# Kernel tuning notes

Hardware: AMD Instinct MI355X
Metric: run time of the kernel (lower is better)

## Reference

```python
import jax, jax.numpy as jnp
import numpy as np

N = 50000   # in_size (nodes)
E = 400000  # edges per network
H = 4       # n_heads
D = 64      # dimension per head
M = 3       # n_modalities


def setup_inputs() -> dict:
    key = jax.random.key(0)
    ks = jax.random.split(key, 10)
    return {
        "x": jax.random.normal(ks[0], (N, H * D), dtype=jnp.float32),
        "edge_index_0": jax.random.randint(ks[1], (2, E), 0, N, dtype=jnp.int32),
        "edge_index_1": jax.random.randint(ks[2], (2, E), 0, N, dtype=jnp.int32),
        "edge_index_2": jax.random.randint(ks[3], (2, E), 0, N, dtype=jnp.int32),
        "attn_0": jax.random.uniform(ks[4], (E, H), dtype=jnp.float32),
        "attn_1": jax.random.uniform(ks[5], (E, H), dtype=jnp.float32),
        "attn_2": jax.random.uniform(ks[6], (E, H), dtype=jnp.float32),
        "net_weights": jax.random.uniform(ks[7], (M,), dtype=jnp.float32),
        "lin_weight": jax.random.normal(ks[8], (H * D, H * D), dtype=jnp.float32) * (1.0 / np.sqrt(H * D)),
        "bias": jnp.zeros((H * D,), dtype=jnp.float32),
    }


def reference(x, edge_index_0, edge_index_1, edge_index_2,
              attn_0, attn_1, attn_2, net_weights, lin_weight, bias):
    # --- aggregat_edge_weights: per-network scalar weight * per-edge attention,
    # combined into one sparse COO attention matrix. Coalescing (summing duplicate
    # edges) is deferred to the scatter-add below, which is mathematically identical.
    edges = jnp.concatenate([edge_index_0, edge_index_1, edge_index_2], axis=1)  # [2, 3E]
    alpha = jnp.concatenate([
        net_weights[0] * attn_0,
        net_weights[1] * attn_1,
        net_weights[2] * attn_2,
    ], axis=0)  # [3E, H]

    # --- CoAttnWGATConv with precomputed alpha (no self-loops):
    # project, reshape to heads, gather source messages, scale by alpha, scatter-sum.
    xp = (x @ lin_weight).reshape(N, H, D)          # [N, H, D]
    src, dst = edges[0], edges[1]
    msgs = xp[src] * alpha[:, :, None]              # [3E, H, D]
    out = jax.ops.segment_sum(msgs, dst, num_segments=N)  # [N, H, D]
    return out.reshape(N, H * D) + bias
```

## Files before the change

### kernel.cpp

```cpp
#include <hip/hip_runtime.h>

#define N_NODES 50000
#define N_EDGES 400000
#define TOT_E   (3 * N_EDGES)
#define CH      256
#define NHEADS  4
#define BUCKET  64

typedef __attribute__((ext_vector_type(8))) short short8v;
typedef __attribute__((ext_vector_type(8))) unsigned short ushort8v;
typedef __attribute__((ext_vector_type(4))) float float4v;

__device__ inline unsigned short f2b(float f) {
  union { float f; unsigned u; } x; x.f = f;
  return (unsigned short)((x.u + 0x7FFFu + ((x.u >> 16) & 1u)) >> 16);
}
__device__ inline float b2f(unsigned short s) {
  union { unsigned u; float f; } x; x.u = ((unsigned)s) << 16;
  return x.f;
}
__device__ inline float h2f(unsigned short s) {
  return (float)__builtin_bit_cast(_Float16, s);
}

__global__ __launch_bounds__(256) void prep_kernel(
    const float* __restrict__ W, unsigned short* __restrict__ WTp,
    int* __restrict__ cursor) {
  int i = blockIdx.x * 256 + threadIdx.x;
  if (i < N_NODES) cursor[i] = 0;
  if (i < 8192) {
    int f = i >> 9, ks = (i >> 6) & 7, l = i & 63;
    int lr = l & 15, lk = l >> 4;
    unsigned short* dst = WTp + (size_t)i * 8;
    #pragma unroll
    for (int j = 0; j < 8; ++j)
      dst[j] = f2b(W[(ks * 32 + lk * 8 + j) * 256 + f * 16 + lr]);
  }
}

__global__ __launch_bounds__(256) void gemm_kernel(
    const float* __restrict__ x, const unsigned short* __restrict__ WTp,
    unsigned short* __restrict__ xpb) {
  const int tid = threadIdx.x;
  const int w = tid >> 6;
  const int l = tid & 63;
  const int lr = l & 15, lk = l >> 4;
  const int xrow = blockIdx.x * 64 + w * 16 + lr;
  const int fbase = blockIdx.y * 4;
  const bool valid = (xrow < N_NODES);
  const short8v* __restrict__ wp = (const short8v*)WTp;

  float4v acc[4];
  #pragma unroll
  for (int f = 0; f < 4; ++f) acc[f] = (float4v)0.0f;

  for (int ks = 0; ks < 8; ++ks) {
    short8v b;
    if (valid) {
      const float4* px = (const float4*)(x + (size_t)xrow * 256 + ks * 32 + lk * 8);
      float4 u0 = px[0], u1 = px[1];
      b[0]=(short)f2b(u0.x); b[1]=(short)f2b(u0.y); b[2]=(short)f2b(u0.z); b[3]=(short)f2b(u0.w);
      b[4]=(short)f2b(u1.x); b[5]=(short)f2b(u1.y); b[6]=(short)f2b(u1.z); b[7]=(short)f2b(u1.w);
    } else {
      b = (short8v)0;
    }
    #pragma unroll
    for (int f = 0; f < 4; ++f) {
      short8v a = wp[((fbase + f) * 8 + ks) * 64 + l];
      acc[f] = __builtin_amdgcn_mfma_f32_16x16x32_bf16(a, b, acc[f], 0, 0, 0);
    }
  }

  if (valid) {
    unsigned short* rowp = xpb + (size_t)xrow * 256 + lk * 4;
    #pragma unroll
    for (int f = 0; f < 4; ++f) {
      ushort4 pk;
      pk.x = f2b(acc[f][0]);
      pk.y = f2b(acc[f][1]);
      pk.z = f2b(acc[f][2]);
      pk.w = f2b(acc[f][3]);
      *(ushort4*)(rowp + (fbase + f) * 16) = pk;
    }
  }
}

__global__ __launch_bounds__(256) void fill_kernel(
    const int* __restrict__ e0, const int* __restrict__ e1,
    const int* __restrict__ e2,
    const float* __restrict__ a0, const float* __restrict__ a1,
    const float* __restrict__ a2, const float* __restrict__ nw,
    int* __restrict__ cursor, int* __restrict__ srcs,
    ushort4* __restrict__ abuf) {
  int g = blockIdx.x * 256 + threadIdx.x;
  if (g >= TOT_E) return;
  int net = (g >= 2 * N_EDGES) ? 2 : (g >= N_EDGES ? 1 : 0);
  int e = g - net * N_EDGES;
  const int* ei = (net == 0) ? e0 : (net == 1 ? e1 : e2);
  const float* at = (net == 0) ? a0 : (net == 1 ? a1 : a2);
  const float wv = nw[net];
  int src = ei[e];
  int dst = ei[N_EDGES + e];
  float4 al = *(const float4*)(at + (size_t)e * NHEADS);
  ushort4 pk;
  pk.x = __builtin_bit_cast(unsigned short, (_Float16)(wv * al.x));
  pk.y = __builtin_bit_cast(unsigned short, (_Float16)(wv * al.y));
  pk.z = __builtin_bit_cast(unsigned short, (_Float16)(wv * al.z));
  pk.w = __builtin_bit_cast(unsigned short, (_Float16)(wv * al.w));
  int pos = atomicAdd(&cursor[dst], 1);
  if (pos < BUCKET) {
    size_t slot = (size_t)dst * BUCKET + pos;
    srcs[slot] = src;
    abuf[slot] = pk;
  }
}

__global__ __launch_bounds__(256) void gather_kernel(
    const int* __restrict__ srcs, const ushort4* __restrict__ abuf,
    const int* __restrict__ cursor,
    const unsigned short* __restrict__ xpb, const float* __restrict__ bias,
    float* __restrict__ out) {
  const int wid = (blockIdx.x * 256 + threadIdx.x) >> 6;
  const int lane = threadIdx.x & 63;
  const int half = lane >> 5;
  const int l = lane & 31;
  const int n = wid * 2 + half;
  const int c = l * 8;
  const int h = l >> 3;

  const int cnt = min(cursor[n], BUCKET);
  const int* __restrict__ sp = srcs + (size_t)n * BUCKET;
  const ushort4* __restrict__ ap = abuf + (size_t)n * BUCKET;

  float acc[8] = {};
  int i = 0;
  for (; i + 4 <= cnt; i += 4) {
    int4 s4 = *(const int4*)(sp + i);
    ushort8v a01 = *(const ushort8v*)(ap + i);
    ushort8v a23 = *(const ushort8v*)(ap + i + 2);
    float A0 = h2f((unsigned short)a01[h]);
    float A1 = h2f((unsigned short)a01[4 + h]);
    float A2 = h2f((unsigned short)a23[h]);
    float A3 = h2f((unsigned short)a23[4 + h]);
    ushort8v v0 = *(const ushort8v*)(xpb + (size_t)s4.x * CH + c);
    ushort8v v1 = *(const ushort8v*)(xpb + (size_t)s4.y * CH + c);
    ushort8v v2 = *(const ushort8v*)(xpb + (size_t)s4.z * CH + c);
    ushort8v v3 = *(const ushort8v*)(xpb + (size_t)s4.w * CH + c);
    #pragma unroll
    for (int j = 0; j < 8; ++j) {
      acc[j] += A0 * b2f(v0[j]) + A1 * b2f(v1[j]) +
                A2 * b2f(v2[j]) + A3 * b2f(v3[j]);
    }
  }
  for (; i < cnt; ++i) {
    int s = sp[i];
    ushort4 av = ap[i];
    float A = h2f((h & 2) ? ((h & 1) ? av.w : av.z) : ((h & 1) ? av.y : av.x));
    ushort8v v = *(const ushort8v*)(xpb + (size_t)s * CH + c);
    #pragma unroll
    for (int j = 0; j < 8; ++j) acc[j] += A * b2f(v[j]);
  }

  const float4 b0 = *(const float4*)(bias + c);
  const float4 b1 = *(const float4*)(bias + c + 4);
  float* o = out + (size_t)n * CH + c;
  *(float4*)(o + 0) = make_float4(acc[0] + b0.x, acc[1] + b0.y, acc[2] + b0.z, acc[3] + b0.w);
  *(float4*)(o + 4) = make_float4(acc[4] + b1.x, acc[5] + b1.y, acc[6] + b1.z, acc[7] + b1.w);
}

extern "C" void kernel_launch(void* const* d_in, const int* in_sizes, int n_in,
                              void* d_out, int out_size, void* d_ws, size_t ws_size,
                              hipStream_t stream) {
  const float* x    = (const float*)d_in[0];
  const int*   e0   = (const int*)d_in[1];
  const int*   e1   = (const int*)d_in[2];
  const int*   e2   = (const int*)d_in[3];
  const float* a0   = (const float*)d_in[4];
  const float* a1   = (const float*)d_in[5];
  const float* a2   = (const float*)d_in[6];
  const float* nw   = (const float*)d_in[7];
  const float* W    = (const float*)d_in[8];
  const float* bias = (const float*)d_in[9];
  float* out = (float*)d_out;

  char* ws = (char*)d_ws;
  size_t o = 0;
  unsigned short* xpb = (unsigned short*)(ws + o); o += (size_t)N_NODES * CH * 2;
  int* srcs      = (int*)(ws + o);                 o += (size_t)N_NODES * BUCKET * 4;
  ushort4* abuf  = (ushort4*)(ws + o);             o += (size_t)N_NODES * BUCKET * 8;
  unsigned short* WTp = (unsigned short*)(ws + o); o += 65536 * 2;
  int* cursor    = (int*)(ws + o);                 o += (size_t)N_NODES * 4;

  const int nNodeBlk = (N_NODES + 255) / 256;
  const int nEdgeBlk = (TOT_E + 255) / 256;

  prep_kernel<<<nNodeBlk, 256, 0, stream>>>(W, WTp, cursor);
  gemm_kernel<<<dim3((N_NODES + 63) / 64, 4), 256, 0, stream>>>(x, WTp, xpb);
  fill_kernel<<<nEdgeBlk, 256, 0, stream>>>(e0, e1, e2, a0, a1, a2, nw,
                                            cursor, srcs, abuf);
  gather_kernel<<<N_NODES / 8, 256, 0, stream>>>(
      srcs, abuf, cursor, xpb, bias, out);
}
```

Measured before the change: 212.8 us.

## Fuse edge bucketing and projection GEMM into one launch with packed edge records

Merges the edge fill kernel and the bf16 MFMA projection GEMM into a single launch that splits work by block index, so the latency-bound atomic bucketing can overlap with the compute-bound GEMM. Source index and fp16 attention weights are packed into one 16-byte record per slot, so the gather does one vector load per edge instead of separate index and attention loads. Cursor zeroing moves to hipMemsetAsync and the prep kernel shrinks to the weight repack only. In exchange, the record buffer is larger because of a padding word, and the fused blocks differ in register needs, which may reduce occupancy.

```diff
diff --git a/kernel.cpp b/kernel.cpp
--- a/kernel.cpp
+++ b/kernel.cpp
@@ -6,6 +6,9 @@
 #define CH      256
 #define NHEADS  4
 #define BUCKET  64
+
+#define FILL_BLOCKS ((TOT_E + 255) / 256)
+#define GEMM_BLOCKS (((N_NODES + 63) / 64) * 4)
 
 typedef __attribute__((ext_vector_type(8))) short short8v;
 typedef __attribute__((ext_vector_type(8))) unsigned short ushort8v;
@@ -22,102 +25,97 @@
 __device__ inline float h2f(unsigned short s) {
   return (float)__builtin_bit_cast(_Float16, s);
 }
+__device__ inline unsigned short f2h(float f) {
+  return __builtin_bit_cast(unsigned short, (_Float16)f);
+}
 
 __global__ __launch_bounds__(256) void prep_kernel(
-    const float* __restrict__ W, unsigned short* __restrict__ WTp,
-    int* __restrict__ cursor) {
+    const float* __restrict__ W, unsigned short* __restrict__ WTp) {
   int i = blockIdx.x * 256 + threadIdx.x;
-  if (i < N_NODES) cursor[i] = 0;
-  if (i < 8192) {
-    int f = i >> 9, ks = (i >> 6) & 7, l = i & 63;
-    int lr = l & 15, lk = l >> 4;
-    unsigned short* dst = WTp + (size_t)i * 8;
-    #pragma unroll
-    for (int j = 0; j < 8; ++j)
-      dst[j] = f2b(W[(ks * 32 + lk * 8 + j) * 256 + f * 16 + lr]);
-  }
+  int f = i >> 9, ks = (i >> 6) & 7, l = i & 63;
+  int lr = l & 15, lk = l >> 4;
+  unsigned short* dst = WTp + (size_t)i * 8;
+  #pragma unroll
+  for (int j = 0; j < 8; ++j)
+    dst[j] = f2b(W[(ks * 32 + lk * 8 + j) * 256 + f * 16 + lr]);
 }
 
-__global__ __launch_bounds__(256) void gemm_kernel(
+__global__ __launch_bounds__(256) void fused_kernel(
+    const int* __restrict__ e0, const int* __restrict__ e1,
+    const int* __restrict__ e2,
+    const float* __restrict__ a0, const float* __restrict__ a1,
+    const float* __restrict__ a2, const float* __restrict__ nw,
+    int* __restrict__ cursor, int4* __restrict__ recs,
     const float* __restrict__ x, const unsigned short* __restrict__ WTp,
     unsigned short* __restrict__ xpb) {
-  const int tid = threadIdx.x;
-  const int w = tid >> 6;
-  const int l = tid & 63;
-  const int lr = l & 15, lk = l >> 4;
-  const int xrow = blockIdx.x * 64 + w * 16 + lr;
-  const int fbase = blockIdx.y * 4;
-  const bool valid = (xrow < N_NODES);
-  const short8v* __restrict__ wp = (const short8v*)WTp;
+  if (blockIdx.x < FILL_BLOCKS) {
+    int g = blockIdx.x * 256 + threadIdx.x;
+    if (g >= TOT_E) return;
+    int net = (g >= 2 * N_EDGES) ? 2 : (g >= N_EDGES ? 1 : 0);
+    int e = g - net * N_EDGES;
+    const int* ei = (net == 0) ? e0 : (net == 1 ? e1 : e2);
+    const float* at = (net == 0) ? a0 : (net == 1 ? a1 : a2);
+    const float wv = nw[net];
+    int src = ei[e];
+    int dst = ei[N_EDGES + e];
+    float4 al = *(const float4*)(at + (size_t)e * NHEADS);
+    int4 rec;
+    rec.x = src;
+    rec.y = ((int)f2h(wv * al.y) << 16) | (int)f2h(wv * al.x);
+    rec.z = ((int)f2h(wv * al.w) << 16) | (int)f2h(wv * al.z);
+    rec.w = 0;
+    int pos = atomicAdd(&cursor[dst], 1);
+    if (pos < BUCKET) recs[(size_t)dst * BUCKET + pos] = rec;
+  } else {
+    const int gb = blockIdx.x - FILL_BLOCKS;
+    const int fbase = (gb & 3) * 4;
+    const int xtile = gb >> 2;
+    const int tid = threadIdx.x;
+    const int w = tid >> 6;
+    const int l = tid & 63;
+    const int lr = l & 15, lk = l >> 4;
+    const int xrow = xtile * 64 + w * 16 + lr;
+    const bool valid = (xrow < N_NODES);
+    const short8v* __restrict__ wp = (const short8v*)WTp;
 
-  float4v acc[4];
-  #pragma unroll
-  for (int f = 0; f < 4; ++f) acc[f] = (float4v)0.0f;
+    float4v acc[4];
+    #pragma unroll
+    for (int f = 0; f < 4; ++f) acc[f] = (float4v)0.0f;
 
-  for (int ks = 0; ks < 8; ++ks) {
-    short8v b;
+    for (int ks = 0; ks < 8; ++ks) {
+      short8v b;
+      if (valid) {
+        const float4* px = (const float4*)(x + (size_t)xrow * 256 + ks * 32 + lk * 8);
+        float4 u0 = px[0], u1 = px[1];
+        b[0]=(short)f2b(u0.x); b[1]=(short)f2b(u0.y); b[2]=(short)f2b(u0.z); b[3]=(short)f2b(u0.w);
+        b[4]=(short)f2b(u1.x); b[5]=(short)f2b(u1.y); b[6]=(short)f2b(u1.z); b[7]=(short)f2b(u1.w);
+      } else {
+        b = (short8v)0;
+      }
+      #pragma unroll
+      for (int f = 0; f < 4; ++f) {
+        short8v a = wp[((fbase + f) * 8 + ks) * 64 + l];
+        acc[f] = __builtin_amdgcn_mfma_f32_16x16x32_bf16(a, b, acc[f], 0, 0, 0);
+      }
+    }
+
     if (valid) {
-      const float4* px = (const float4*)(x + (size_t)xrow * 256 + ks * 32 + lk * 8);
-      float4 u0 = px[0], u1 = px[1];
-      b[0]=(short)f2b(u0.x); b[1]=(short)f2b(u0.y); b[2]=(short)f2b(u0.z); b[3]=(short)f2b(u0.w);
-      b[4]=(short)f2b(u1.x); b[5]=(short)f2b(u1.y); b[6]=(short)f2b(u1.z); b[7]=(short)f2b(u1.w);
-    } else {
-      b = (short8v)0;
-    }
-    #pragma unroll
-    for (int f = 0; f < 4; ++f) {
-      short8v a = wp[((fbase + f) * 8 + ks) * 64 + l];
-      acc[f] = __builtin_amdgcn_mfma_f32_16x16x32_bf16(a, b, acc[f], 0, 0, 0);
-    }
-  }
-
-  if (valid) {
-    unsigned short* rowp = xpb + (size_t)xrow * 256 + lk * 4;
-    #pragma unroll
-    for (int f = 0; f < 4; ++f) {
-      ushort4 pk;
-      pk.x = f2b(acc[f][0]);
-      pk.y = f2b(acc[f][1]);
-      pk.z = f2b(acc[f][2]);
-      pk.w = f2b(acc[f][3]);
-      *(ushort4*)(rowp + (fbase + f) * 16) = pk;
+      unsigned short* rowp = xpb + (size_t)xrow * 256 + lk * 4;
+      #pragma unroll
+      for (int f = 0; f < 4; ++f) {
+        ushort4 pk;
+        pk.x = f2b(acc[f][0]);
+        pk.y = f2b(acc[f][1]);
+        pk.z = f2b(acc[f][2]);
+        pk.w = f2b(acc[f][3]);
+        *(ushort4*)(rowp + (fbase + f) * 16) = pk;
+      }
     }
   }
 }
 
-__global__ __launch_bounds__(256) void fill_kernel(
-    const int* __restrict__ e0, const int* __restrict__ e1,
-    const int* __restrict__ e2,
-    const float* __restrict__ a0, const float* __restrict__ a1,
-    const float* __restrict__ a2, const float* __restrict__ nw,
-    int* __restrict__ cursor, int* __restrict__ srcs,
-    ushort4* __restrict__ abuf) {
-  int g = blockIdx.x * 256 + threadIdx.x;
-  if (g >= TOT_E) return;
-  int net = (g >= 2 * N_EDGES) ? 2 : (g >= N_EDGES ? 1 : 0);
-  int e = g - net * N_EDGES;
-  const int* ei = (net == 0) ? e0 : (net == 1 ? e1 : e2);
-  const float* at = (net == 0) ? a0 : (net == 1 ? a1 : a2);
-  const float wv = nw[net];
-  int src = ei[e];
-  int dst = ei[N_EDGES + e];
-  float4 al = *(const float4*)(at + (size_t)e * NHEADS);
-  ushort4 pk;
-  pk.x = __builtin_bit_cast(unsigned short, (_Float16)(wv * al.x));
-  pk.y = __builtin_bit_cast(unsigned short, (_Float16)(wv * al.y));
-  pk.z = __builtin_bit_cast(unsigned short, (_Float16)(wv * al.z));
-  pk.w = __builtin_bit_cast(unsigned short, (_Float16)(wv * al.w));
-  int pos = atomicAdd(&cursor[dst], 1);
-  if (pos < BUCKET) {
-    size_t slot = (size_t)dst * BUCKET + pos;
-    srcs[slot] = src;
-    abuf[slot] = pk;
-  }
-}
-
 __global__ __launch_bounds__(256) void gather_kernel(
-    const int* __restrict__ srcs, const ushort4* __restrict__ abuf,
-    const int* __restrict__ cursor,
+    const int4* __restrict__ recs, const int* __restrict__ cursor,
     const unsigned short* __restrict__ xpb, const float* __restrict__ bias,
     float* __restrict__ out) {
   const int wid = (blockIdx.x * 256 + threadIdx.x) >> 6;
@@ -129,23 +127,24 @@
   const int h = l >> 3;
 
   const int cnt = min(cursor[n], BUCKET);
-  const int* __restrict__ sp = srcs + (size_t)n * BUCKET;
-  const ushort4* __restrict__ ap = abuf + (size_t)n * BUCKET;
+  const int4* __restrict__ rp = recs + (size_t)n * BUCKET;
 
   float acc[8] = {};
   int i = 0;
   for (; i + 4 <= cnt; i += 4) {
-    int4 s4 = *(const int4*)(sp + i);
-    ushort8v a01 = *(const ushort8v*)(ap + i);
-    ushort8v a23 = *(const ushort8v*)(ap + i + 2);
-    float A0 = h2f((unsigned short)a01[h]);
-    float A1 = h2f((unsigned short)a01[4 + h]);
-    float A2 = h2f((unsigned short)a23[h]);
-    float A3 = h2f((unsigned short)a23[4 + h]);
-    ushort8v v0 = *(const ushort8v*)(xpb + (size_t)s4.x * CH + c);
-    ushort8v v1 = *(const ushort8v*)(xpb + (size_t)s4.y * CH + c);
-    ushort8v v2 = *(const ushort8v*)(xpb + (size_t)s4.z * CH + c);
-    ushort8v v3 = *(const ushort8v*)(xpb + (size_t)s4.w * CH + c);
+    int4 r0 = rp[i + 0], r1 = rp[i + 1], r2 = rp[i + 2], r3 = rp[i + 3];
+    unsigned w0 = (h & 2) ? (unsigned)r0.z : (unsigned)r0.y;
+    unsigned w1 = (h & 2) ? (unsigned)r1.z : (unsigned)r1.y;
+    unsigned w2 = (h & 2) ? (unsigned)r2.z : (unsigned)r2.y;
+    unsigned w3 = (h & 2) ? (unsigned)r3.z : (unsigned)r3.y;
+    float A0 = h2f((unsigned short)((h & 1) ? (w0 >> 16) : (w0 & 0xffff)));
+    float A1 = h2f((unsigned short)((h & 1) ? (w1 >> 16) : (w1 & 0xffff)));
+    float A2 = h2f((unsigned short)((h & 1) ? (w2 >> 16) : (w2 & 0xffff)));
+    float A3 = h2f((unsigned short)((h & 1) ? (w3 >> 16) : (w3 & 0xffff)));
+    ushort8v v0 = *(const ushort8v*)(xpb + (size_t)r0.x * CH + c);
+    ushort8v v1 = *(const ushort8v*)(xpb + (size_t)r1.x * CH + c);
+    ushort8v v2 = *(const ushort8v*)(xpb + (size_t)r2.x * CH + c);
+    ushort8v v3 = *(const ushort8v*)(xpb + (size_t)r3.x * CH + c);
     #pragma unroll
     for (int j = 0; j < 8; ++j) {
       acc[j] += A0 * b2f(v0[j]) + A1 * b2f(v1[j]) +
@@ -153,10 +152,10 @@
     }
   }
   for (; i < cnt; ++i) {
-    int s = sp[i];
-    ushort4 av = ap[i];
-    float A = h2f((h & 2) ? ((h & 1) ? av.w : av.z) : ((h & 1) ? av.y : av.x));
-    ushort8v v = *(const ushort8v*)(xpb + (size_t)s * CH + c);
+    int4 r = rp[i];
+    unsigned wd = (h & 2) ? (unsigned)r.z : (unsigned)r.y;
+    float A = h2f((unsigned short)((h & 1) ? (wd >> 16) : (wd & 0xffff)));
+    ushort8v v = *(const ushort8v*)(xpb + (size_t)r.x * CH + c);
     #pragma unroll
     for (int j = 0; j < 8; ++j) acc[j] += A * b2f(v[j]);
   }
@@ -186,18 +185,13 @@
   char* ws = (char*)d_ws;
   size_t o = 0;
   unsigned short* xpb = (unsigned short*)(ws + o); o += (size_t)N_NODES * CH * 2;
-  int* srcs      = (int*)(ws + o);                 o += (size_t)N_NODES * BUCKET * 4;
-  ushort4* abuf  = (ushort4*)(ws + o);             o += (size_t)N_NODES * BUCKET * 8;
+  int4* recs = (int4*)(ws + o);                    o += (size_t)N_NODES * BUCKET * 16;
   unsigned short* WTp = (unsigned short*)(ws + o); o += 65536 * 2;
-  int* cursor    = (int*)(ws + o);                 o += (size_t)N_NODES * 4;
+  int* cursor = (int*)(ws + o);                    o += (size_t)N_NODES * 4;
 
-  const int nNodeBlk = (N_NODES + 255) / 256;
-  const int nEdgeBlk = (TOT_E + 255) / 256;
-
-  prep_kernel<<<nNodeBlk, 256, 0, stream>>>(W, WTp, cursor);
-  gemm_kernel<<<dim3((N_NODES + 63) / 64, 4), 256, 0, stream>>>(x, WTp, xpb);
-  fill_kernel<<<nEdgeBlk, 256, 0, stream>>>(e0, e1, e2, a0, a1, a2, nw,
-                                            cursor, srcs, abuf);
-  gather_kernel<<<N_NODES / 8, 256, 0, stream>>>(
-      srcs, abuf, cursor, xpb, bias, out);
+  hipMemsetAsync(cursor, 0, (size_t)N_NODES * 4, stream);
+  prep_kernel<<<32, 256, 0, stream>>>(W, WTp);
+  fused_kernel<<<FILL_BLOCKS + GEMM_BLOCKS, 256, 0, stream>>>(
+      e0, e1, e2, a0, a1, a2, nw, cursor, recs, x, WTp, xpb);
+  gather_kernel<<<N_NODES / 8, 256, 0, stream>>>(recs, cursor, xpb, bias, out);
 }
```

Measured after the change: 215.4 us. Within noise of the previous version (+1.2%).
